# Performance work log

Measured on AMD Instinct MI355X. Metric: run time of the kernel, lower is better.

Reference implementation:

```python
import jax, jax.numpy as jnp
import numpy as np

NHEAD = 8


def _global_query_attention(cs, ks, vs):
    """cs: (B,H,G,Ek) global queries; ks: (B,H,S,Ek); vs: (B,H,S,Ev).
    For each key position i: v'_i = sum_{s<=i} softmax(K[:i] @ q) * V[:i].
    Returns (B,H,S,G,Ev)."""
    w = jnp.exp(jnp.einsum('bhge,bhse->bhgs', cs, ks))          # (B,H,G,S)
    norms = jnp.cumsum(w, axis=-1)                               # (B,H,G,S)
    wv = w[..., None] * vs[:, :, None, :, :]                     # (B,H,G,S,Ev) -- huge intermediate
    resp = jnp.cumsum(wv, axis=-2) / norms[..., None]            # (B,H,G,S,Ev)
    return jnp.swapaxes(resp, -3, -2)                            # (B,H,S,G,Ev)


def setup_inputs() -> dict:
    B, L, E, G = 4, 2048, 512, 16
    KD = VD = E
    keys = jax.random.split(jax.random.key(0), 9)
    s_qk = 0.02              # keep exp(q.k) finite in fp32
    s_v = 1.0 / np.sqrt(VD).astype(np.float32)
    return {
        'query':        jax.random.normal(keys[0], (B, L, E), jnp.float32),
        'key':          jax.random.normal(keys[1], (B, L, E), jnp.float32),
        'value':        jax.random.normal(keys[2], (B, L, E), jnp.float32),
        'context':      jax.random.normal(keys[3], (B, G, E), jnp.float32),
        'query_proj':   jax.random.normal(keys[4], (1, E, KD), jnp.float32) * s_qk,
        'key_proj':     jax.random.normal(keys[5], (1, E, KD), jnp.float32) * s_qk,
        'value_proj':   jax.random.normal(keys[6], (1, E, VD), jnp.float32) * s_v,
        'output_proj':  jax.random.normal(keys[7], (1, VD, E), jnp.float32) * s_v,
        'context_proj': jax.random.normal(keys[8], (1, E, KD), jnp.float32) * s_qk,
    }


def reference(query, key, value, context, query_proj, key_proj, value_proj, output_proj, context_proj):
    B, L, E = query.shape
    G = context.shape[1]
    H = NHEAD
    KD = query_proj.shape[-1]
    VD = value_proj.shape[-1]
    Ek, Ev = KD // H, VD // H

    def heads(x, W, n, dh):
        # (B,n,E) @ (1,E,D) -> (B,n,D) -> (B,H,n,dh)
        return jnp.swapaxes((x @ W).reshape(B, n, H, dh), 1, 2)

    cs = heads(context, context_proj, G, Ek)   # (B,H,G,Ek)
    qs = heads(query, query_proj, L, Ek)       # (B,H,L,Ek)
    ks = heads(key, key_proj, L, Ek)           # (B,H,S,Ek)
    vs = heads(value, value_proj, L, Ev)       # (B,H,S,Ev)

    resp_v = _global_query_attention(cs, ks, vs)   # (B,H,S,G,Ev)
    resp_k = _global_query_attention(cs, ks, ks)   # (B,H,S,G,Ek)

    logits = jnp.einsum('bhse,bhsge->bhsg', qs, resp_k)   # (B,H,S,G)
    w = jax.nn.softmax(logits, axis=-1)
    out = jnp.einsum('bhsg,bhsge->bhse', w, resp_v)       # (B,H,S,Ev)
    out = jnp.swapaxes(out, 1, 2).reshape(B, L, VD)       # (B,S,vdim)
    return out @ output_proj                               # (B,S,d_model)
```

## Files before the change

### kernel.cpp

```cpp
#include <hip/hip_runtime.h>
#include <hip/hip_bf16.h>

#define NB 4
#define SL 2048
#define NG 16
#define NH 8
#define DH 64
#define NBH (NB * NH)
#define NCH (SL / 64)

typedef __attribute__((ext_vector_type(8))) short bh8;
typedef __attribute__((ext_vector_type(4))) float fx4;

__device__ __forceinline__ ushort f2bf(float x) {
    union { float f; unsigned u; } v; v.f = x;
    const unsigned r = v.u + 0x7fffu + ((v.u >> 16) & 1u);
    return (ushort)(r >> 16);
}
__device__ __forceinline__ float b2f(ushort u) {
    union { unsigned u; float f; } v; v.u = ((unsigned)u) << 16;
    return v.f;
}
__device__ __forceinline__ bh8 pack8(float4 lo, float4 hi) {
    bh8 r;
    r[0] = (short)f2bf(lo.x); r[1] = (short)f2bf(lo.y);
    r[2] = (short)f2bf(lo.z); r[3] = (short)f2bf(lo.w);
    r[4] = (short)f2bf(hi.x); r[5] = (short)f2bf(hi.y);
    r[6] = (short)f2bf(hi.z); r[7] = (short)f2bf(hi.w);
    return r;
}
__device__ __forceinline__ void unpack8(bh8 v, float4& lo, float4& hi) {
    lo.x = b2f((ushort)v[0]); lo.y = b2f((ushort)v[1]);
    lo.z = b2f((ushort)v[2]); lo.w = b2f((ushort)v[3]);
    hi.x = b2f((ushort)v[4]); hi.y = b2f((ushort)v[5]);
    hi.z = b2f((ushort)v[6]); hi.w = b2f((ushort)v[7]);
}
__device__ __forceinline__ int swz(int row, int col) {
    return row * 64 + (col ^ ((row & 7) << 3));
}

__global__ __launch_bounds__(256) void prep_kernel(
    const float* __restrict__ w0, const float* __restrict__ w1,
    const float* __restrict__ w2, const float* __restrict__ w3,
    const float* __restrict__ cp, const float* __restrict__ context,
    ushort* __restrict__ o0, ushort* __restrict__ o1,
    ushort* __restrict__ o2, ushort* __restrict__ o3,
    float* __restrict__ cs) {
    const int z = blockIdx.z;
    const int t = threadIdx.x;
    if (z < 4) {
        const float* W = (z == 0) ? w0 : (z == 1) ? w1 : (z == 2) ? w2 : w3;
        ushort* WT = (z == 0) ? o0 : (z == 1) ? o1 : (z == 2) ? o2 : o3;
        __shared__ float tile[32][33];
        const int bx = blockIdx.x * 32, by = blockIdx.y * 32;
        const int tx = t & 31, ty = t >> 5;
#pragma unroll
        for (int p = 0; p < 4; ++p)
            tile[ty + p * 8][tx] = W[(size_t)(by + ty + p * 8) * 512 + bx + tx];
        __syncthreads();
#pragma unroll
        for (int p = 0; p < 4; ++p)
            WT[(size_t)(bx + ty + p * 8) * 512 + by + tx] = f2bf(tile[tx][ty + p * 8]);
    } else {
        if (blockIdx.x != 0 || blockIdx.y >= 8) return;
        __shared__ float As[16][65];
        __shared__ float Bs[16][64];
        const int cn = blockIdx.y * 64;
        const int tm = t >> 4, tn = t & 15;
        const int arow = t >> 2, ak = (t & 3) << 2;
        const int bk = t >> 4, bc = (t & 15) << 2;
        float acc[4][4] = {};
        for (int k0 = 0; k0 < 512; k0 += 16) {
            float4 av = *(const float4*)&context[(size_t)arow * 512 + k0 + ak];
            float4 bv = *(const float4*)&cp[(size_t)(k0 + bk) * 512 + cn + bc];
            __syncthreads();
            As[ak + 0][arow] = av.x;
            As[ak + 1][arow] = av.y;
            As[ak + 2][arow] = av.z;
            As[ak + 3][arow] = av.w;
            *(float4*)&Bs[bk][bc] = bv;
            __syncthreads();
#pragma unroll
            for (int kk = 0; kk < 16; ++kk) {
                float a0 = As[kk][tm * 4 + 0], a1 = As[kk][tm * 4 + 1];
                float a2 = As[kk][tm * 4 + 2], a3 = As[kk][tm * 4 + 3];
                float4 b = *(const float4*)&Bs[kk][tn * 4];
                acc[0][0] += a0 * b.x; acc[0][1] += a0 * b.y; acc[0][2] += a0 * b.z; acc[0][3] += a0 * b.w;
                acc[1][0] += a1 * b.x; acc[1][1] += a1 * b.y; acc[1][2] += a1 * b.z; acc[1][3] += a1 * b.w;
                acc[2][0] += a2 * b.x; acc[2][1] += a2 * b.y; acc[2][2] += a2 * b.z; acc[2][3] += a2 * b.w;
                acc[3][0] += a3 * b.x; acc[3][1] += a3 * b.y; acc[3][2] += a3 * b.z; acc[3][3] += a3 * b.w;
            }
        }
#pragma unroll
        for (int j = 0; j < 4; ++j) {
            const int r = tm * 4 + j;
#pragma unroll
            for (int jj = 0; jj < 4; ++jj) {
                const int cc = cn + tn * 4 + jj;
                const int b = r / NG, i = r % NG;
                cs[(((size_t)(b * NH) + (cc >> 6)) * NG + i) * DH + (cc & 63)] = acc[j][jj];
            }
        }
    }
}

__global__ __launch_bounds__(256, 3) void gemm_qkv_kernel(
    const float* __restrict__ qf, const float* __restrict__ kf,
    const float* __restrict__ vf, const ushort* __restrict__ qpT,
    const ushort* __restrict__ kpT, const ushort* __restrict__ vpT,
    ushort* __restrict__ qsb, ushort* __restrict__ ksb, ushort* __restrict__ vsb) {
    const int z = blockIdx.z;
    const float* A32 = (z == 0) ? qf : (z == 1) ? kf : vf;
    const ushort* BT = (z == 0) ? qpT : (z == 1) ? kpT : vpT;
    ushort* out = (z == 0) ? qsb : (z == 1) ? ksb : vsb;

    __shared__ __align__(16) ushort As[2][64 * 64];
    __shared__ __align__(16) ushort Bs[2][128 * 64];
    const int t = threadIdx.x;
    const int lane = t & 63, w = t >> 6;
    const int bm = blockIdx.x * 64, bn = blockIdx.y * 128;
    const int ar = t >> 2, ao = (t & 3) * 16;
    const size_t abase = (size_t)(bm + ar) * 512 + ao;
    const int asw0 = swz(ar, ao), asw1 = swz(ar, ao + 8);
    size_t bsrc[4];
#pragma unroll
    for (int i = 0; i < 4; ++i) {
        const int s = w * 2048 + i * 512 + lane * 8;
        const int r = s >> 6, o = (s & 63) ^ ((r & 7) << 3);
        bsrc[i] = (size_t)(bn + r) * 512 + o;
    }
    const int wr = w >> 1, wc = w & 1;
    const int fr = lane & 15, kg = lane >> 4;
    fx4 acc[2][4] = {};
    float4 a0v, a1v, a2v, a3v;

#define LOADA(kk)                                                              \
    do {                                                                       \
        a0v = *(const float4*)&A32[abase + (kk)];                              \
        a1v = *(const float4*)&A32[abase + (kk) + 4];                          \
        a2v = *(const float4*)&A32[abase + (kk) + 8];                          \
        a3v = *(const float4*)&A32[abase + (kk) + 12];                         \
    } while (0)
#define WRITEA(buf)                                                            \
    do {                                                                       \
        *(bh8*)&As[buf][asw0] = pack8(a0v, a1v);                               \
        *(bh8*)&As[buf][asw1] = pack8(a2v, a3v);                               \
    } while (0)
#define STAGEB(buf, kk)                                                        \
    do {                                                                       \
        _Pragma("unroll")                                                      \
        for (int i = 0; i < 4; ++i)                                            \
            __builtin_amdgcn_global_load_lds(                                  \
                (const __attribute__((address_space(1))) void*)(BT + bsrc[i] + (kk)), \
                (__attribute__((address_space(3))) void*)&Bs[buf][w * 2048 + i * 512], \
                16, 0, 0);                                                     \
    } while (0)
#define MFMA_PHASE(buf)                                                        \
    do {                                                                       \
        _Pragma("unroll")                                                      \
        for (int kk = 0; kk < 2; ++kk) {                                       \
            bh8 af[2], bf[4];                                                  \
            _Pragma("unroll")                                                  \
            for (int m = 0; m < 2; ++m) {                                      \
                const int R = wr * 32 + m * 16 + fr;                           \
                af[m] = *(const bh8*)&As[buf][swz(R, kk * 32 + kg * 8)];       \
            }                                                                  \
            _Pragma("unroll")                                                  \
            for (int nn = 0; nn < 4; ++nn) {                                   \
                const int C = wc * 64 + nn * 16 + fr;                          \
                bf[nn] = *(const bh8*)&Bs[buf][swz(C, kk * 32 + kg * 8)];      \
            }                                                                  \
            _Pragma("unroll")                                                  \
            for (int m = 0; m < 2; ++m)                                        \
                _Pragma("unroll")                                              \
                for (int nn = 0; nn < 4; ++nn)                                 \
                    acc[m][nn] = __builtin_amdgcn_mfma_f32_16x16x32_bf16(      \
                        af[m], bf[nn], acc[m][nn], 0, 0, 0);                   \
        }                                                                      \
    } while (0)

    LOADA(0);
    STAGEB(0, 0);
    WRITEA(0);
    STAGEB(1, 64);
    LOADA(64);
    asm volatile("s_waitcnt vmcnt(8) lgkmcnt(0)" ::: "memory");
    __builtin_amdgcn_s_barrier();
    __builtin_amdgcn_sched_barrier(0);

    int cur = 0;
    for (int k0 = 0; k0 < 512; k0 += 64) {
        MFMA_PHASE(cur);
        if (k0 + 64 < 512) WRITEA(cur ^ 1);
        asm volatile("s_waitcnt lgkmcnt(0)" ::: "memory");
        __builtin_amdgcn_s_barrier();
        __builtin_amdgcn_sched_barrier(0);
        if (k0 + 128 < 512) {
            STAGEB(cur, k0 + 128);
            LOADA(k0 + 128);
            asm volatile("s_waitcnt vmcnt(8)" ::: "memory");
        } else if (k0 + 64 < 512) {
            asm volatile("s_waitcnt vmcnt(0)" ::: "memory");
        }
        __builtin_amdgcn_sched_barrier(0);
        cur ^= 1;
    }
#undef LOADA
#undef WRITEA
#undef STAGEB
#undef MFMA_PHASE
#pragma unroll
    for (int m = 0; m < 2; ++m)
#pragma unroll
        for (int nn = 0; nn < 4; ++nn)
#pragma unroll
            for (int j = 0; j < 4; ++j) {
                const int r = bm + wr * 32 + m * 16 + kg * 4 + j;
                const int cc = bn + wc * 64 + nn * 16 + fr;
                const int b = r >> 11, i = r & 2047;
                out[(((size_t)(b * NH) + (cc >> 6)) * SL + i) * DH + (cc & 63)] =
                    f2bf(acc[m][nn][j]);
            }
}

__global__ __launch_bounds__(256, 3) void gemm_out_kernel(const ushort* __restrict__ A,
                                                          const ushort* __restrict__ BT,
                                                          float* __restrict__ out) {
    __shared__ __align__(16) ushort As[2][64 * 64];
    __shared__ __align__(16) ushort Bs[2][128 * 64];
    const int t = threadIdx.x;
    const int lane = t & 63, w = t >> 6;
    const int bm = blockIdx.x * 64, bn = blockIdx.y * 128;
    size_t asrc[2], bsrc[4];
#pragma unroll
    for (int i = 0; i < 2; ++i) {
        const int s = w * 1024 + i * 512 + lane * 8;
        const int r = s >> 6, o = (s & 63) ^ ((r & 7) << 3);
        asrc[i] = (size_t)(bm + r) * 512 + o;
    }
#pragma unroll
    for (int i = 0; i < 4; ++i) {
        const int s = w * 2048 + i * 512 + lane * 8;
        const int r = s >> 6, o = (s & 63) ^ ((r & 7) << 3);
        bsrc[i] = (size_t)(bn + r) * 512 + o;
    }
    const int wr = w >> 1, wc = w & 1;
    const int fr = lane & 15, kg = lane >> 4;
    fx4 acc[2][4] = {};

#define STAGE_O(buf, kk)                                                       \
    do {                                                                       \
        _Pragma("unroll")                                                      \
        for (int i = 0; i < 2; ++i)                                            \
            __builtin_amdgcn_global_load_lds(                                  \
                (const __attribute__((address_space(1))) void*)(A + asrc[i] + (kk)), \
                (__attribute__((address_space(3))) void*)&As[buf][w * 1024 + i * 512], \
                16, 0, 0);                                                     \
        _Pragma("unroll")                                                      \
        for (int i = 0; i < 4; ++i)                                            \
            __builtin_amdgcn_global_load_lds(                                  \
                (const __attribute__((address_space(1))) void*)(BT + bsrc[i] + (kk)), \
                (__attribute__((address_space(3))) void*)&Bs[buf][w * 2048 + i * 512], \
                16, 0, 0);                                                     \
    } while (0)

    STAGE_O(0, 0);
    STAGE_O(1, 64);
    asm volatile("s_waitcnt vmcnt(6)" ::: "memory");
    __builtin_amdgcn_s_barrier();
    __builtin_amdgcn_sched_barrier(0);
    int cur = 0;
    for (int k0 = 0; k0 < 512; k0 += 64) {
#pragma unroll
        for (int kk = 0; kk < 2; ++kk) {
            bh8 af[2], bf[4];
#pragma unroll
            for (int m = 0; m < 2; ++m) {
                const int R = wr * 32 + m * 16 + fr;
                af[m] = *(const bh8*)&As[cur][swz(R, kk * 32 + kg * 8)];
            }
#pragma unroll
            for (int nn = 0; nn < 4; ++nn) {
                const int C = wc * 64 + nn * 16 + fr;
                bf[nn] = *(const bh8*)&Bs[cur][swz(C, kk * 32 + kg * 8)];
            }
#pragma unroll
            for (int m = 0; m < 2; ++m)
#pragma unroll
                for (int nn = 0; nn < 4; ++nn)
                    acc[m][nn] = __builtin_amdgcn_mfma_f32_16x16x32_bf16(
                        af[m], bf[nn], acc[m][nn], 0, 0, 0);
        }
        asm volatile("s_waitcnt lgkmcnt(0)" ::: "memory");
        __builtin_amdgcn_s_barrier();
        __builtin_amdgcn_sched_barrier(0);
        if (k0 + 128 < 512) {
            STAGE_O(cur, k0 + 128);
            asm volatile("s_waitcnt vmcnt(6)" ::: "memory");
        } else if (k0 + 64 < 512) {
            asm volatile("s_waitcnt vmcnt(0)" ::: "memory");
        }
        __builtin_amdgcn_sched_barrier(0);
        cur ^= 1;
    }
#undef STAGE_O
#pragma unroll
    for (int m = 0; m < 2; ++m)
#pragma unroll
        for (int nn = 0; nn < 4; ++nn)
#pragma unroll
            for (int j = 0; j < 4; ++j) {
                const int r = bm + wr * 32 + m * 16 + kg * 4 + j;
                const int cc = bn + wc * 64 + nn * 16 + fr;
                out[(size_t)r * 512 + cc] = acc[m][nn][j];
            }
}

__global__ __launch_bounds__(256) void chunk_sums_w_kernel(
    const ushort* __restrict__ ksb, const ushort* __restrict__ vsb,
    const float* __restrict__ cs, float* __restrict__ wb,
    float* __restrict__ wbT, float* __restrict__ Mc, float* __restrict__ Nc) {
    const int bh = blockIdx.x, c = blockIdx.y;
    __shared__ float Ks[64 * 64];
    __shared__ float Vs[64 * 64];
    __shared__ float Ws[64 * 16];
    __shared__ float Cs[16][65];
    const int t = threadIdx.x;
    const ushort* kbase = ksb + ((size_t)bh * SL + c * 64) * DH;
    const ushort* vbase = vsb + ((size_t)bh * SL + c * 64) * DH;
#pragma unroll
    for (int p = 0; p < 2; ++p) {
        const int idx = (p * 256 + t) * 8;
        float4 lo, hi;
        unpack8(*(const bh8*)&kbase[idx], lo, hi);
        *(float4*)&Ks[idx] = lo; *(float4*)&Ks[idx + 4] = hi;
        unpack8(*(const bh8*)&vbase[idx], lo, hi);
        *(float4*)&Vs[idx] = lo; *(float4*)&Vs[idx + 4] = hi;
    }
    {
        const int idx = t * 4;
        const float4 cv = *(const float4*)&cs[(size_t)bh * NG * DH + idx];
        const int g = idx >> 6, e = idx & 63;
        Cs[g][e + 0] = cv.x; Cs[g][e + 1] = cv.y; Cs[g][e + 2] = cv.z; Cs[g][e + 3] = cv.w;
    }
    __syncthreads();
    {
        const int i = (t * 4) >> 4, g0 = (t * 4) & 15;
        float d0 = 0.f, d1 = 0.f, d2 = 0.f, d3 = 0.f;
#pragma unroll 8
        for (int e = 0; e < 64; ++e) {
            const float kv = Ks[i * 64 + e];
            d0 += kv * Cs[g0 + 0][e];
            d1 += kv * Cs[g0 + 1][e];
            d2 += kv * Cs[g0 + 2][e];
            d3 += kv * Cs[g0 + 3][e];
        }
        float4 wv;
        wv.x = expf(d0); wv.y = expf(d1); wv.z = expf(d2); wv.w = expf(d3);
        *(float4*)&Ws[i * 16 + g0] = wv;
        *(float4*)&wb[((size_t)bh * SL + c * 64 + i) * NG + g0] = wv;
    }
    __syncthreads();
    {
        const int g = t >> 4, i0 = (t & 15) * 4;
        float4 wv4;
        wv4.x = Ws[(i0 + 0) * 16 + g];
        wv4.y = Ws[(i0 + 1) * 16 + g];
        wv4.z = Ws[(i0 + 2) * 16 + g];
        wv4.w = Ws[(i0 + 3) * 16 + g];
        *(float4*)&wbT[((size_t)(bh * NG) + g) * SL + c * 64 + i0] = wv4;
    }
    const int e = t >> 2, g0 = (t & 3) * 4;
    float m0 = 0.f, m1 = 0.f, m2 = 0.f, m3 = 0.f;
#pragma unroll 8
    for (int i = 0; i < 64; ++i) {
        const float kv = Ks[i * 64 + e];
        const float4 w = *(const float4*)&Ws[i * 16 + g0];
        m0 += kv * w.x; m1 += kv * w.y; m2 += kv * w.z; m3 += kv * w.w;
    }
    const int g2 = t >> 4, e2 = (t & 15) * 4;
    float n0 = 0.f, n1 = 0.f, n2 = 0.f, n3 = 0.f;
#pragma unroll 8
    for (int i = 0; i < 64; ++i) {
        const float wv = Ws[i * 16 + g2];
        const float4 vv = *(const float4*)&Vs[i * 64 + e2];
        n0 += wv * vv.x; n1 += wv * vv.y; n2 += wv * vv.z; n3 += wv * vv.w;
    }
    float* mo = Mc + ((size_t)(bh * NCH + c) * 64 + e) * 16 + g0;
    mo[0] = m0; mo[1] = m1; mo[2] = m2; mo[3] = m3;
    float* no = Nc + ((size_t)(bh * NCH + c) * 16 + g2) * 64 + e2;
    no[0] = n0; no[1] = n1; no[2] = n2; no[3] = n3;
}

__global__ __launch_bounds__(256) void scans_kernel(const float* __restrict__ wbT,
                                                    float* __restrict__ nb,
                                                    float* __restrict__ Mc,
                                                    float* __restrict__ Nc) {
    const int bid = blockIdx.x;
    const int t = threadIdx.x;
    if (bid < NBH * NG) {
        __shared__ float sw[2048];
        __shared__ float sp[256];
#pragma unroll
        for (int p = 0; p < 2; ++p) {
            const int idx = (p * 256 + t) * 4;
            *(float4*)&sw[idx] = *(const float4*)&wbT[(size_t)bid * SL + idx];
        }
        __syncthreads();
        float loc[8];
        float run = 0.f;
#pragma unroll
        for (int j = 0; j < 8; ++j) { run += sw[t * 8 + j]; loc[j] = run; }
        sp[t] = run;
        __syncthreads();
        for (int off = 1; off < 256; off <<= 1) {
            const float v = sp[t];
            const float add = (t >= off) ? sp[t - off] : 0.f;
            __syncthreads();
            sp[t] = v + add;
            __syncthreads();
        }
        const float offs = (t > 0) ? sp[t - 1] : 0.f;
#pragma unroll
        for (int j = 0; j < 8; ++j)
            nb[(size_t)bid * SL + t * 8 + j] = offs + loc[j];
    } else {
        const int idx = bid - NBH * NG;
        const int bh = idx >> 1;
        float* base = ((idx & 1) ? Nc : Mc) + (size_t)bh * NCH * 1024;
        float4 run = make_float4(0.f, 0.f, 0.f, 0.f);
        float4 nxt = *(float4*)&base[t * 4];
        for (int c = 0; c < NCH; ++c) {
            const float4 v = nxt;
            if (c + 1 < NCH) nxt = *(float4*)&base[(c + 1) * 1024 + t * 4];
            *(float4*)&base[c * 1024 + t * 4] = run;
            run.x += v.x; run.y += v.y; run.z += v.z; run.w += v.w;
        }
    }
}

__global__ __launch_bounds__(256) void pass1c_kernel(const ushort* __restrict__ qsb,
                                                     const ushort* __restrict__ ksb,
                                                     const float* __restrict__ wb,
                                                     const float* __restrict__ nb,
                                                     const float* __restrict__ Mc,
                                                     float* __restrict__ cb) {
    const int bh = blockIdx.x;
    const int r = blockIdx.y;
    const int s0 = r * 64;
    __shared__ float Qs[64][65];
    __shared__ float Kt[64][65];
    __shared__ float At[64][65];
    __shared__ float Wt[64 * 16];
    __shared__ float Pt[64 * 16];
    __shared__ float Lg[64][17];
    const int t = threadIdx.x;
    const int am = t >> 4, an = t & 15;
    const ushort* qbase = qsb + ((size_t)bh * SL + s0) * DH;
    const ushort* kbase = ksb + ((size_t)bh * SL + s0) * DH;
#pragma unroll
    for (int p = 0; p < 2; ++p) {
        const int idx = (p * 256 + t) * 8;
        const int row = idx >> 6, col = idx & 63;
        float4 lo, hi;
        unpack8(*(const bh8*)&qbase[idx], lo, hi);
        *(float4*)&Qs[row][col] = lo; *(float4*)&Qs[row][col + 4] = hi;
        unpack8(*(const bh8*)&kbase[idx], lo, hi);
        *(float4*)&Kt[row][col] = lo; *(float4*)&Kt[row][col + 4] = hi;
    }
    *(float4*)&Wt[t * 4] = *(const float4*)&wb[((size_t)bh * SL + s0) * NG + t * 4];
    *(float4*)&Pt[t * 4] = *(const float4*)&Mc[(size_t)(bh * NCH + r) * 1024 + t * 4];
    __syncthreads();
    float a[4][4] = {};
#pragma unroll 8
    for (int e = 0; e < 64; ++e) {
        float qv[4], kv[4];
#pragma unroll
        for (int j = 0; j < 4; ++j) qv[j] = Qs[am * 4 + j][e];
#pragma unroll
        for (int jj = 0; jj < 4; ++jj) kv[jj] = Kt[an * 4 + jj][e];
#pragma unroll
        for (int j = 0; j < 4; ++j)
#pragma unroll
            for (int jj = 0; jj < 4; ++jj) a[j][jj] += qv[j] * kv[jj];
    }
#pragma unroll
    for (int j = 0; j < 4; ++j)
#pragma unroll
        for (int jj = 0; jj < 4; ++jj) {
            if (an * 4 + jj > am * 4 + j) a[j][jj] = 0.f;
            At[am * 4 + j][an * 4 + jj] = a[j][jj];
        }
    __syncthreads();
    float lg[4] = {0.f, 0.f, 0.f, 0.f};
#pragma unroll 8
    for (int ii = 0; ii < 64; ++ii) {
        const float wv = Wt[ii * 16 + an];
#pragma unroll
        for (int j = 0; j < 4; ++j) lg[j] += At[am * 4 + j][ii] * wv;
    }
#pragma unroll 8
    for (int e = 0; e < 64; ++e) {
        const float pv = Pt[e * 16 + an];
#pragma unroll
        for (int j = 0; j < 4; ++j) lg[j] += Qs[am * 4 + j][e] * pv;
    }
#pragma unroll
    for (int j = 0; j < 4; ++j) Lg[am * 4 + j][an] = lg[j];
    __syncthreads();
    if (t < 64) {
        const int s = s0 + t;
        const float* nbase = nb + (size_t)bh * NG * SL + s;
        float nv[16], l[16];
        float mx = -1e30f;
#pragma unroll
        for (int g = 0; g < 16; ++g) {
            nv[g] = nbase[(size_t)g * SL];
            l[g] = Lg[t][g] / nv[g];
            mx = fmaxf(mx, l[g]);
        }
        float sum = 0.f;
#pragma unroll
        for (int g = 0; g < 16; ++g) { l[g] = expf(l[g] - mx); sum += l[g]; }
        const float inv = 1.f / sum;
#pragma unroll
        for (int g = 0; g < 16; ++g)
            cb[((size_t)bh * SL + s) * NG + g] = l[g] * inv / nv[g];
    }
}

__global__ __launch_bounds__(256) void pass2c_kernel(const float* __restrict__ cb,
                                                     const float* __restrict__ wb,
                                                     const ushort* __restrict__ vsb,
                                                     const float* __restrict__ Nc,
                                                     ushort* __restrict__ ohb) {
    const int bh = blockIdx.x;
    const int b = bh >> 3, h = bh & 7;
    const int r = blockIdx.y;
    const int s0 = r * 64;
    __shared__ float Ct[64][17];
    __shared__ float Wt[64][17];
    __shared__ float Vt[64 * 64];
    __shared__ float St[64][65];
    __shared__ float Ut[16 * 64];
    const int t = threadIdx.x;
    const int am = t >> 4, an = t & 15;
    {
        const int idx = t * 4;
        const int row = idx >> 4, g0 = idx & 15;
        const float4 cv = *(const float4*)&cb[((size_t)bh * SL + s0) * NG + idx];
        Ct[row][g0 + 0] = cv.x; Ct[row][g0 + 1] = cv.y;
        Ct[row][g0 + 2] = cv.z; Ct[row][g0 + 3] = cv.w;
        const float4 wv = *(const float4*)&wb[((size_t)bh * SL + s0) * NG + idx];
        Wt[row][g0 + 0] = wv.x; Wt[row][g0 + 1] = wv.y;
        Wt[row][g0 + 2] = wv.z; Wt[row][g0 + 3] = wv.w;
    }
    const ushort* vbase = vsb + ((size_t)bh * SL + s0) * DH;
#pragma unroll
    for (int p = 0; p < 2; ++p) {
        const int idx = (p * 256 + t) * 8;
        float4 lo, hi;
        unpack8(*(const bh8*)&vbase[idx], lo, hi);
        *(float4*)&Vt[idx] = lo; *(float4*)&Vt[idx + 4] = hi;
    }
    *(float4*)&Ut[t * 4] = *(const float4*)&Nc[(size_t)(bh * NCH + r) * 1024 + t * 4];
    __syncthreads();
    float sv[4][4] = {};
#pragma unroll
    for (int g = 0; g < 16; ++g) {
        float cv[4], wv[4];
#pragma unroll
        for (int j = 0; j < 4; ++j) cv[j] = Ct[am * 4 + j][g];
#pragma unroll
        for (int jj = 0; jj < 4; ++jj) wv[jj] = Wt[an * 4 + jj][g];
#pragma unroll
        for (int j = 0; j < 4; ++j)
#pragma unroll
            for (int jj = 0; jj < 4; ++jj) sv[j][jj] += cv[j] * wv[jj];
    }
#pragma unroll
    for (int j = 0; j < 4; ++j)
#pragma unroll
        for (int jj = 0; jj < 4; ++jj) {
            if (an * 4 + jj > am * 4 + j) sv[j][jj] = 0.f;
            St[am * 4 + j][an * 4 + jj] = sv[j][jj];
        }
    __syncthreads();
    float acc[4][4] = {};
#pragma unroll
    for (int g = 0; g < 16; ++g) {
        const float4 u = *(const float4*)&Ut[g * 64 + an * 4];
        float cv[4];
#pragma unroll
        for (int j = 0; j < 4; ++j) cv[j] = Ct[am * 4 + j][g];
#pragma unroll
        for (int j = 0; j < 4; ++j) {
            acc[j][0] += cv[j] * u.x; acc[j][1] += cv[j] * u.y;
            acc[j][2] += cv[j] * u.z; acc[j][3] += cv[j] * u.w;
        }
    }
#pragma unroll 8
    for (int ii = 0; ii < 64; ++ii) {
        const float4 vv = *(const float4*)&Vt[ii * 64 + an * 4];
        float st[4];
#pragma unroll
        for (int j = 0; j < 4; ++j) st[j] = St[am * 4 + j][ii];
#pragma unroll
        for (int j = 0; j < 4; ++j) {
            acc[j][0] += st[j] * vv.x; acc[j][1] += st[j] * vv.y;
            acc[j][2] += st[j] * vv.z; acc[j][3] += st[j] * vv.w;
        }
    }
#pragma unroll
    for (int j = 0; j < 4; ++j) {
        const int s = s0 + am * 4 + j;
        ushort4 pk;
        pk.x = f2bf(acc[j][0]); pk.y = f2bf(acc[j][1]);
        pk.z = f2bf(acc[j][2]); pk.w = f2bf(acc[j][3]);
        *(ushort4*)&ohb[((size_t)b * SL + s) * 512 + h * DH + an * 4] = pk;
    }
}

extern "C" void kernel_launch(void* const* d_in, const int* in_sizes, int n_in,
                              void* d_out, int out_size, void* d_ws, size_t ws_size,
                              hipStream_t stream) {
    const float* query   = (const float*)d_in[0];
    const float* key     = (const float*)d_in[1];
    const float* value   = (const float*)d_in[2];
    const float* context = (const float*)d_in[3];
    const float* qp = (const float*)d_in[4];
    const float* kp = (const float*)d_in[5];
    const float* vp = (const float*)d_in[6];
    const float* op = (const float*)d_in[7];
    const float* cp = (const float*)d_in[8];
    float* out = (float*)d_out;

    ushort* qsb = (ushort*)d_ws;
    ushort* ksb = qsb + 4194304;
    ushort* vsb = ksb + 4194304;
    ushort* ohb = vsb + 4194304;
    ushort* qpT = ohb + 4194304;
    ushort* kpT = qpT + 262144;
    ushort* vpT = kpT + 262144;
    ushort* opT = vpT + 262144;
    float* fbase = (float*)(opT + 262144);
    float* cs = fbase;
    float* wb = cs + 32768;
    float* nb = wb + 1048576;
    float* Mc = nb + 1048576;
    float* Nc = Mc + 1048576;
    float* cb = Nc + 1048576;
    float* wbT = cb + 1048576;

    dim3 blk(256);
    prep_kernel<<<dim3(16, 16, 5), blk, 0, stream>>>(qp, kp, vp, op, cp, context,
                                                     qpT, kpT, vpT, opT, cs);
    gemm_qkv_kernel<<<dim3(128, 4, 3), blk, 0, stream>>>(query, key, value,
                                                         qpT, kpT, vpT, qsb, ksb, vsb);
    chunk_sums_w_kernel<<<dim3(NBH, NCH), blk, 0, stream>>>(ksb, vsb, cs, wb, wbT, Mc, Nc);
    scans_kernel<<<dim3(NBH * NG + NBH * 2), blk, 0, stream>>>(wbT, nb, Mc, Nc);
    pass1c_kernel<<<dim3(NBH, NCH), blk, 0, stream>>>(qsb, ksb, wb, nb, Mc, cb);
    pass2c_kernel<<<dim3(NBH, NCH), blk, 0, stream>>>(cb, wb, vsb, Nc, ohb);
    gemm_out_kernel<<<dim3(128, 4), blk, 0, stream>>>(ohb, opT, out);
}
```

Before: 145.4 us.

## Keep full A row-block resident in LDS and sweep all N tiles in QKV GEMM

The QKV projection GEMM now converts a 32-row block of the fp32 input to bf16 once, holds the whole K=512 extent in LDS, and loops over all four 128-column output tiles. Only B tiles are streamed through the double buffer. This removes the repeated fp32 reads and conversion of A that the old 64x128 tiling did once per N tile, at the cost of more LDS per block (occupancy hint lowered to 2) and a smaller M tile per wave. The context-projection branch of prep_kernel is also rewritten as a simpler 32-block kernel that keeps the context rows in shared memory and reads the projection weights directly.

```diff
diff --git a/kernel.cpp b/kernel.cpp
--- a/kernel.cpp
+++ b/kernel.cpp
@@ -48,179 +48,147 @@
     float* __restrict__ cs) {
     const int z = blockIdx.z;
     const int t = threadIdx.x;
+    __shared__ float smem[16 * 512];
     if (z < 4) {
         const float* W = (z == 0) ? w0 : (z == 1) ? w1 : (z == 2) ? w2 : w3;
         ushort* WT = (z == 0) ? o0 : (z == 1) ? o1 : (z == 2) ? o2 : o3;
-        __shared__ float tile[32][33];
+        float* tile = smem;
         const int bx = blockIdx.x * 32, by = blockIdx.y * 32;
         const int tx = t & 31, ty = t >> 5;
 #pragma unroll
         for (int p = 0; p < 4; ++p)
-            tile[ty + p * 8][tx] = W[(size_t)(by + ty + p * 8) * 512 + bx + tx];
+            tile[(ty + p * 8) * 33 + tx] = W[(size_t)(by + ty + p * 8) * 512 + bx + tx];
         __syncthreads();
 #pragma unroll
         for (int p = 0; p < 4; ++p)
-            WT[(size_t)(bx + ty + p * 8) * 512 + by + tx] = f2bf(tile[tx][ty + p * 8]);
+            WT[(size_t)(bx + ty + p * 8) * 512 + by + tx] = f2bf(tile[tx * 33 + ty + p * 8]);
     } else {
-        if (blockIdx.x != 0 || blockIdx.y >= 8) return;
-        __shared__ float As[16][65];
-        __shared__ float Bs[16][64];
-        const int cn = blockIdx.y * 64;
-        const int tm = t >> 4, tn = t & 15;
-        const int arow = t >> 2, ak = (t & 3) << 2;
-        const int bk = t >> 4, bc = (t & 15) << 2;
-        float acc[4][4] = {};
-        for (int k0 = 0; k0 < 512; k0 += 16) {
-            float4 av = *(const float4*)&context[(size_t)arow * 512 + k0 + ak];
-            float4 bv = *(const float4*)&cp[(size_t)(k0 + bk) * 512 + cn + bc];
-            __syncthreads();
-            As[ak + 0][arow] = av.x;
-            As[ak + 1][arow] = av.y;
-            As[ak + 2][arow] = av.z;
-            As[ak + 3][arow] = av.w;
-            *(float4*)&Bs[bk][bc] = bv;
-            __syncthreads();
-#pragma unroll
-            for (int kk = 0; kk < 16; ++kk) {
-                float a0 = As[kk][tm * 4 + 0], a1 = As[kk][tm * 4 + 1];
-                float a2 = As[kk][tm * 4 + 2], a3 = As[kk][tm * 4 + 3];
-                float4 b = *(const float4*)&Bs[kk][tn * 4];
-                acc[0][0] += a0 * b.x; acc[0][1] += a0 * b.y; acc[0][2] += a0 * b.z; acc[0][3] += a0 * b.w;
-                acc[1][0] += a1 * b.x; acc[1][1] += a1 * b.y; acc[1][2] += a1 * b.z; acc[1][3] += a1 * b.w;
-                acc[2][0] += a2 * b.x; acc[2][1] += a2 * b.y; acc[2][2] += a2 * b.z; acc[2][3] += a2 * b.w;
-                acc[3][0] += a3 * b.x; acc[3][1] += a3 * b.y; acc[3][2] += a3 * b.z; acc[3][3] += a3 * b.w;
-            }
+        if (blockIdx.x >= 8 || blockIdx.y >= 4) return;
+        const int ngc = blockIdx.x;
+        const int mg = blockIdx.y;
+        const int sr = t >> 4, sc0 = (t & 15) * 32;
+#pragma unroll
+        for (int i = 0; i < 8; ++i)
+            *(float4*)&smem[sr * 512 + sc0 + i * 4] =
+                *(const float4*)&context[(size_t)(mg * 16 + sr) * 512 + sc0 + i * 4];
+        __syncthreads();
+        const int c = ngc * 64 + (t & 63);
+        const int rg = t >> 6;
+        float acc0 = 0.f, acc1 = 0.f, acc2 = 0.f, acc3 = 0.f;
+#pragma unroll 8
+        for (int e = 0; e < 512; ++e) {
+            const float b = cp[(size_t)e * 512 + c];
+            acc0 += smem[(rg * 4 + 0) * 512 + e] * b;
+            acc1 += smem[(rg * 4 + 1) * 512 + e] * b;
+            acc2 += smem[(rg * 4 + 2) * 512 + e] * b;
+            acc3 += smem[(rg * 4 + 3) * 512 + e] * b;
         }
 #pragma unroll
         for (int j = 0; j < 4; ++j) {
-            const int r = tm * 4 + j;
-#pragma unroll
-            for (int jj = 0; jj < 4; ++jj) {
-                const int cc = cn + tn * 4 + jj;
-                const int b = r / NG, i = r % NG;
-                cs[(((size_t)(b * NH) + (cc >> 6)) * NG + i) * DH + (cc & 63)] = acc[j][jj];
-            }
-        }
-    }
-}
-
-__global__ __launch_bounds__(256, 3) void gemm_qkv_kernel(
+            const float v = (j == 0) ? acc0 : (j == 1) ? acc1 : (j == 2) ? acc2 : acc3;
+            const int m = mg * 16 + rg * 4 + j;
+            const int b = m >> 4, i = m & 15;
+            cs[(((size_t)(b * NH) + (c >> 6)) * NG + i) * DH + (c & 63)] = v;
+        }
+    }
+}
+
+__global__ __launch_bounds__(256, 2) void gemm_qkv_kernel(
     const float* __restrict__ qf, const float* __restrict__ kf,
     const float* __restrict__ vf, const ushort* __restrict__ qpT,
     const ushort* __restrict__ kpT, const ushort* __restrict__ vpT,
     ushort* __restrict__ qsb, ushort* __restrict__ ksb, ushort* __restrict__ vsb) {
-    const int z = blockIdx.z;
+    const int z = blockIdx.y;
     const float* A32 = (z == 0) ? qf : (z == 1) ? kf : vf;
     const ushort* BT = (z == 0) ? qpT : (z == 1) ? kpT : vpT;
     ushort* out = (z == 0) ? qsb : (z == 1) ? ksb : vsb;
 
-    __shared__ __align__(16) ushort As[2][64 * 64];
+    __shared__ __align__(16) ushort As[8 * 2048];
     __shared__ __align__(16) ushort Bs[2][128 * 64];
     const int t = threadIdx.x;
     const int lane = t & 63, w = t >> 6;
-    const int bm = blockIdx.x * 64, bn = blockIdx.y * 128;
-    const int ar = t >> 2, ao = (t & 3) * 16;
-    const size_t abase = (size_t)(bm + ar) * 512 + ao;
-    const int asw0 = swz(ar, ao), asw1 = swz(ar, ao + 8);
-    size_t bsrc[4];
+    const int bm = blockIdx.x * 32;
+    const int arow = t >> 3, achk = t & 7;
+    {
+        const float* ap = A32 + (size_t)(bm + arow) * 512 + achk * 64;
+#pragma unroll
+        for (int i = 0; i < 8; ++i) {
+            const float4 lo = *(const float4*)&ap[i * 8];
+            const float4 hi = *(const float4*)&ap[i * 8 + 4];
+            *(bh8*)&As[achk * 2048 + swz(arow, i * 8)] = pack8(lo, hi);
+        }
+    }
+    int rB[4], oB[4];
 #pragma unroll
     for (int i = 0; i < 4; ++i) {
         const int s = w * 2048 + i * 512 + lane * 8;
-        const int r = s >> 6, o = (s & 63) ^ ((r & 7) << 3);
-        bsrc[i] = (size_t)(bn + r) * 512 + o;
+        rB[i] = s >> 6;
+        oB[i] = (s & 63) ^ ((rB[i] & 7) << 3);
     }
     const int wr = w >> 1, wc = w & 1;
     const int fr = lane & 15, kg = lane >> 4;
-    fx4 acc[2][4] = {};
-    float4 a0v, a1v, a2v, a3v;
-
-#define LOADA(kk)                                                              \
+    fx4 acc[4] = {};
+
+#define STAGE_B(buf, p)                                                        \
     do {                                                                       \
-        a0v = *(const float4*)&A32[abase + (kk)];                              \
-        a1v = *(const float4*)&A32[abase + (kk) + 4];                          \
-        a2v = *(const float4*)&A32[abase + (kk) + 8];                          \
-        a3v = *(const float4*)&A32[abase + (kk) + 12];                         \
-    } while (0)
-#define WRITEA(buf)                                                            \
-    do {                                                                       \
-        *(bh8*)&As[buf][asw0] = pack8(a0v, a1v);                               \
-        *(bh8*)&As[buf][asw1] = pack8(a2v, a3v);                               \
-    } while (0)
-#define STAGEB(buf, kk)                                                        \
-    do {                                                                       \
+        const int bn_ = (p) >> 3, k0_ = ((p) & 7) * 64;                        \
         _Pragma("unroll")                                                      \
         for (int i = 0; i < 4; ++i)                                            \
             __builtin_amdgcn_global_load_lds(                                  \
-                (const __attribute__((address_space(1))) void*)(BT + bsrc[i] + (kk)), \
+                (const __attribute__((address_space(1))) void*)                \
+                    (BT + (size_t)(bn_ * 128 + rB[i]) * 512 + k0_ + oB[i]),    \
                 (__attribute__((address_space(3))) void*)&Bs[buf][w * 2048 + i * 512], \
                 16, 0, 0);                                                     \
     } while (0)
-#define MFMA_PHASE(buf)                                                        \
-    do {                                                                       \
-        _Pragma("unroll")                                                      \
-        for (int kk = 0; kk < 2; ++kk) {                                       \
-            bh8 af[2], bf[4];                                                  \
-            _Pragma("unroll")                                                  \
-            for (int m = 0; m < 2; ++m) {                                      \
-                const int R = wr * 32 + m * 16 + fr;                           \
-                af[m] = *(const bh8*)&As[buf][swz(R, kk * 32 + kg * 8)];       \
-            }                                                                  \
-            _Pragma("unroll")                                                  \
-            for (int nn = 0; nn < 4; ++nn) {                                   \
-                const int C = wc * 64 + nn * 16 + fr;                          \
-                bf[nn] = *(const bh8*)&Bs[buf][swz(C, kk * 32 + kg * 8)];      \
-            }                                                                  \
-            _Pragma("unroll")                                                  \
-            for (int m = 0; m < 2; ++m)                                        \
-                _Pragma("unroll")                                              \
-                for (int nn = 0; nn < 4; ++nn)                                 \
-                    acc[m][nn] = __builtin_amdgcn_mfma_f32_16x16x32_bf16(      \
-                        af[m], bf[nn], acc[m][nn], 0, 0, 0);                   \
-        }                                                                      \
-    } while (0)
-
-    LOADA(0);
-    STAGEB(0, 0);
-    WRITEA(0);
-    STAGEB(1, 64);
-    LOADA(64);
-    asm volatile("s_waitcnt vmcnt(8) lgkmcnt(0)" ::: "memory");
+
+    STAGE_B(0, 0);
+    STAGE_B(1, 1);
+    asm volatile("s_waitcnt vmcnt(4) lgkmcnt(0)" ::: "memory");
     __builtin_amdgcn_s_barrier();
     __builtin_amdgcn_sched_barrier(0);
 
-    int cur = 0;
-    for (int k0 = 0; k0 < 512; k0 += 64) {
-        MFMA_PHASE(cur);
-        if (k0 + 64 < 512) WRITEA(cur ^ 1);
+    for (int p = 0; p < 32; ++p) {
+        const int buf = p & 1;
+        const int kc = p & 7;
+        const int bn = p >> 3;
+#pragma unroll
+        for (int kk = 0; kk < 2; ++kk) {
+            const int off = kk * 32 + kg * 8;
+            bh8 af = *(const bh8*)&As[kc * 2048 + swz(wr * 16 + fr, off)];
+            bh8 bf[4];
+#pragma unroll
+            for (int nn = 0; nn < 4; ++nn)
+                bf[nn] = *(const bh8*)&Bs[buf][swz(wc * 64 + nn * 16 + fr, off)];
+#pragma unroll
+            for (int nn = 0; nn < 4; ++nn)
+                acc[nn] = __builtin_amdgcn_mfma_f32_16x16x32_bf16(af, bf[nn], acc[nn], 0, 0, 0);
+        }
+        if (kc == 7) {
+#pragma unroll
+            for (int nn = 0; nn < 4; ++nn) {
+#pragma unroll
+                for (int j = 0; j < 4; ++j) {
+                    const int r = bm + wr * 16 + kg * 4 + j;
+                    const int cc = bn * 128 + wc * 64 + nn * 16 + fr;
+                    const int b = r >> 11, i = r & 2047;
+                    out[(((size_t)(b * NH) + (cc >> 6)) * SL + i) * DH + (cc & 63)] =
+                        f2bf(acc[nn][j]);
+                }
+                acc[nn] = (fx4){0.f, 0.f, 0.f, 0.f};
+            }
+        }
         asm volatile("s_waitcnt lgkmcnt(0)" ::: "memory");
         __builtin_amdgcn_s_barrier();
         __builtin_amdgcn_sched_barrier(0);
-        if (k0 + 128 < 512) {
-            STAGEB(cur, k0 + 128);
-            LOADA(k0 + 128);
-            asm volatile("s_waitcnt vmcnt(8)" ::: "memory");
-        } else if (k0 + 64 < 512) {
+        if (p + 2 < 32) {
+            STAGE_B(buf, p + 2);
+            asm volatile("s_waitcnt vmcnt(4)" ::: "memory");
+        } else if (p + 1 < 32) {
             asm volatile("s_waitcnt vmcnt(0)" ::: "memory");
         }
         __builtin_amdgcn_sched_barrier(0);
-        cur ^= 1;
-    }
-#undef LOADA
-#undef WRITEA
-#undef STAGEB
-#undef MFMA_PHASE
-#pragma unroll
-    for (int m = 0; m < 2; ++m)
-#pragma unroll
-        for (int nn = 0; nn < 4; ++nn)
-#pragma unroll
-            for (int j = 0; j < 4; ++j) {
-                const int r = bm + wr * 32 + m * 16 + kg * 4 + j;
-                const int cc = bn + wc * 64 + nn * 16 + fr;
-                const int b = r >> 11, i = r & 2047;
-                out[(((size_t)(b * NH) + (cc >> 6)) * SL + i) * DH + (cc & 63)] =
-                    f2bf(acc[m][nn][j]);
-            }
+    }
+#undef STAGE_B
 }
 
 __global__ __launch_bounds__(256, 3) void gemm_out_kernel(const ushort* __restrict__ A,
@@ -655,8 +623,8 @@
     dim3 blk(256);
     prep_kernel<<<dim3(16, 16, 5), blk, 0, stream>>>(qp, kp, vp, op, cp, context,
                                                      qpT, kpT, vpT, opT, cs);
-    gemm_qkv_kernel<<<dim3(128, 4, 3), blk, 0, stream>>>(query, key, value,
-                                                         qpT, kpT, vpT, qsb, ksb, vsb);
+    gemm_qkv_kernel<<<dim3(256, 3), blk, 0, stream>>>(query, key, value,
+                                                      qpT, kpT, vpT, qsb, ksb, vsb);
     chunk_sums_w_kernel<<<dim3(NBH, NCH), blk, 0, stream>>>(ksb, vsb, cs, wb, wbT, Mc, Nc);
     scans_kernel<<<dim3(NBH * NG + NBH * 2), blk, 0, stream>>>(wbT, nb, Mc, Nc);
     pass1c_kernel<<<dim3(NBH, NCH), blk, 0, stream>>>(qsb, ksb, wb, nb, Mc, cb);
```

Result: slower. 167.6 us (+15.3%).

## Split context projection across 32 blocks instead of 8

Applied to the files above, without the earlier changes.

The context projection inside the prep kernel previously ran on only 8 blocks, each looping over the full K dimension with a tiled shared-memory GEMM. It now uses 32 blocks (8 column groups by 4 row groups). Each block stages a 16x512 slice of the context in shared memory and computes 4 rows per thread while streaming projection columns from global memory. This shortens the serial tail of the prep kernel, at the cost of a larger shared-memory allocation (32KB) that also applies to the transpose blocks and may reduce their occupancy.

```diff
diff --git a/kernel.cpp b/kernel.cpp
--- a/kernel.cpp
+++ b/kernel.cpp
@@ -48,58 +48,47 @@
     float* __restrict__ cs) {
     const int z = blockIdx.z;
     const int t = threadIdx.x;
+    __shared__ float smem[16 * 512];
     if (z < 4) {
         const float* W = (z == 0) ? w0 : (z == 1) ? w1 : (z == 2) ? w2 : w3;
         ushort* WT = (z == 0) ? o0 : (z == 1) ? o1 : (z == 2) ? o2 : o3;
-        __shared__ float tile[32][33];
+        float* tile = smem;
         const int bx = blockIdx.x * 32, by = blockIdx.y * 32;
         const int tx = t & 31, ty = t >> 5;
 #pragma unroll
         for (int p = 0; p < 4; ++p)
-            tile[ty + p * 8][tx] = W[(size_t)(by + ty + p * 8) * 512 + bx + tx];
+            tile[(ty + p * 8) * 33 + tx] = W[(size_t)(by + ty + p * 8) * 512 + bx + tx];
         __syncthreads();
 #pragma unroll
         for (int p = 0; p < 4; ++p)
-            WT[(size_t)(bx + ty + p * 8) * 512 + by + tx] = f2bf(tile[tx][ty + p * 8]);
+            WT[(size_t)(bx + ty + p * 8) * 512 + by + tx] = f2bf(tile[tx * 33 + ty + p * 8]);
     } else {
-        if (blockIdx.x != 0 || blockIdx.y >= 8) return;
-        __shared__ float As[16][65];
-        __shared__ float Bs[16][64];
-        const int cn = blockIdx.y * 64;
-        const int tm = t >> 4, tn = t & 15;
-        const int arow = t >> 2, ak = (t & 3) << 2;
-        const int bk = t >> 4, bc = (t & 15) << 2;
-        float acc[4][4] = {};
-        for (int k0 = 0; k0 < 512; k0 += 16) {
-            float4 av = *(const float4*)&context[(size_t)arow * 512 + k0 + ak];
-            float4 bv = *(const float4*)&cp[(size_t)(k0 + bk) * 512 + cn + bc];
-            __syncthreads();
-            As[ak + 0][arow] = av.x;
-            As[ak + 1][arow] = av.y;
-            As[ak + 2][arow] = av.z;
-            As[ak + 3][arow] = av.w;
-            *(float4*)&Bs[bk][bc] = bv;
-            __syncthreads();
-#pragma unroll
-            for (int kk = 0; kk < 16; ++kk) {
-                float a0 = As[kk][tm * 4 + 0], a1 = As[kk][tm * 4 + 1];
-                float a2 = As[kk][tm * 4 + 2], a3 = As[kk][tm * 4 + 3];
-                float4 b = *(const float4*)&Bs[kk][tn * 4];
-                acc[0][0] += a0 * b.x; acc[0][1] += a0 * b.y; acc[0][2] += a0 * b.z; acc[0][3] += a0 * b.w;
-                acc[1][0] += a1 * b.x; acc[1][1] += a1 * b.y; acc[1][2] += a1 * b.z; acc[1][3] += a1 * b.w;
-                acc[2][0] += a2 * b.x; acc[2][1] += a2 * b.y; acc[2][2] += a2 * b.z; acc[2][3] += a2 * b.w;
-                acc[3][0] += a3 * b.x; acc[3][1] += a3 * b.y; acc[3][2] += a3 * b.z; acc[3][3] += a3 * b.w;
-            }
+        if (blockIdx.x >= 8 || blockIdx.y >= 4) return;
+        const int ngc = blockIdx.x;
+        const int mg = blockIdx.y;
+        const int sr = t >> 4, sc0 = (t & 15) * 32;
+#pragma unroll
+        for (int i = 0; i < 8; ++i)
+            *(float4*)&smem[sr * 512 + sc0 + i * 4] =
+                *(const float4*)&context[(size_t)(mg * 16 + sr) * 512 + sc0 + i * 4];
+        __syncthreads();
+        const int c = ngc * 64 + (t & 63);
+        const int rg = t >> 6;
+        float acc0 = 0.f, acc1 = 0.f, acc2 = 0.f, acc3 = 0.f;
+#pragma unroll 8
+        for (int e = 0; e < 512; ++e) {
+            const float b = cp[(size_t)e * 512 + c];
+            acc0 += smem[(rg * 4 + 0) * 512 + e] * b;
+            acc1 += smem[(rg * 4 + 1) * 512 + e] * b;
+            acc2 += smem[(rg * 4 + 2) * 512 + e] * b;
+            acc3 += smem[(rg * 4 + 3) * 512 + e] * b;
         }
 #pragma unroll
         for (int j = 0; j < 4; ++j) {
-            const int r = tm * 4 + j;
-#pragma unroll
-            for (int jj = 0; jj < 4; ++jj) {
-                const int cc = cn + tn * 4 + jj;
-                const int b = r / NG, i = r % NG;
-                cs[(((size_t)(b * NH) + (cc >> 6)) * NG + i) * DH + (cc & 63)] = acc[j][jj];
-            }
+            const float v = (j == 0) ? acc0 : (j == 1) ? acc1 : (j == 2) ? acc2 : acc3;
+            const int m = mg * 16 + rg * 4 + j;
+            const int b = m >> 4, i = m & 15;
+            cs[(((size_t)(b * NH) + (c >> 6)) * NG + i) * DH + (c & 63)] = v;
         }
     }
 }
```

After: 141.1 us. -2.9%, faster.
